# Kernel optimization log

Hardware: AMD Instinct MI355X
Metric: run time of the kernel (lower is better)

Reference implementation:

```python
import jax, jax.numpy as jnp
import numpy as np

MD_S = 1
MD_R = 16
EVAL_STEPS = 7
INV_T = 100.0
EPS = 1e-6

B, C, S = 16, 512, 4096  # batch, channels, flattened spatial


def setup_inputs() -> dict:
    key = jax.random.key(0)
    k1, k2 = jax.random.split(key)
    x = jax.random.uniform(k1, (B, C, S), dtype=jnp.float32)  # non-negative input for NMF
    bases = jax.random.uniform(k2, (B * MD_S, S, MD_R), dtype=jnp.float32)
    # F.normalize(bases, dim=1)
    bases = bases / (jnp.linalg.norm(bases, axis=1, keepdims=True) + 1e-12)
    return {"x": x, "bases": bases}


def _nmf_step(xm, bases, coef):
    # xm: (BS, D, N), bases: (BS, D, R), coef: (BS, N, R)
    # multiplicative update for coef
    num = jnp.einsum('bdn,bdr->bnr', xm, bases)
    den = jnp.einsum('bnr,brs->bns', coef, jnp.einsum('bdr,bds->brs', bases, bases))
    coef = coef * num / (den + EPS)
    # multiplicative update for bases
    num = jnp.einsum('bdn,bnr->bdr', xm, coef)
    den = jnp.einsum('bdr,brs->bds', bases, jnp.einsum('bnr,bns->brs', coef, coef))
    bases = bases * num / (den + EPS)
    return bases, coef


def _local_inference(xm, bases):
    # coef init: softmax(inv_t * x^T bases)
    coef = jax.nn.softmax(INV_T * jnp.einsum('bdn,bdr->bnr', xm, bases), axis=-1)

    def body(carry, _):
        b, c = _nmf_step(xm, carry[0], carry[1])
        return (b, c), None

    (bases, coef), _ = jax.lax.scan(body, (bases, coef), None, length=EVAL_STEPS)
    return bases, coef


def reference(x, bases):
    Bb, Cc, Ss = x.shape
    D = Ss
    N = Cc // MD_S
    xm = x.reshape(Bb * MD_S, N, D).transpose(0, 2, 1)  # (BS, D, N)

    bases_i, coef_i = jax.lax.stop_gradient(_local_inference(xm, bases))

    # compute_coef (differentiable in the original module)
    num = jnp.einsum('bdn,bdr->bnr', xm, bases_i)
    den = jnp.einsum('bnr,brs->bns', coef_i, jnp.einsum('bdr,bds->brs', bases_i, bases_i))
    coef = coef_i * num / (den + EPS)

    # x_rec = bases @ coef^T -> (BS, D, N) -> transpose -> (B, C, S)
    out = jnp.einsum('bdr,bnr->bdn', bases_i, coef)
    out = out.transpose(0, 2, 1).reshape(Bb, Cc, Ss)
    return out
```

## Files before the change

kernel.cpp:

```cpp
#include <hip/hip_runtime.h>

#define EPS 1e-6f

template <int CTRL>
__device__ __forceinline__ float dpp_add(float v) {
  int moved = __builtin_amdgcn_update_dpp(0, __float_as_int(v), CTRL, 0xF, 0xF, false);
  return v + __int_as_float(moved);
}

__global__ __launch_bounds__(512, 4) void kernelA(
    const float* __restrict__ x, const float* __restrict__ bases,
    float* __restrict__ Ppart, float* __restrict__ CtC)
{
  __shared__ __align__(16) float lb[512 * 20];
  const int tid = threadIdx.x;
  const int grp = blockIdx.x;
  const int b = blockIdx.y;
  const int h = blockIdx.z;
  if (h == 0 && grp == 0 && tid < 256) CtC[b * 256 + tid] = 0.0f;
  const int w = tid >> 6;
  const int lane = tid & 63;
  const int rg = w & 3;
  const int rh = w >> 2;
  const int n0 = grp * 32 + rg * 8;
  const float* __restrict__ xp = x + ((size_t)(b * 512 + n0)) * 4096 + h * 2048;
  const float4* __restrict__ srcf4 =
      (const float4*)(bases + ((size_t)(b * 4096 + h * 2048)) * 16);

  float acc[8][8];
#pragma unroll
  for (int i = 0; i < 8; ++i)
#pragma unroll
    for (int r = 0; r < 8; ++r) acc[i][r] = 0.0f;

  for (int c = 0; c < 4; ++c) {
#pragma unroll
    for (int k = 0; k < 4; ++k) {
      int idx = k * 512 + tid;
      int dl = idx >> 2, q = idx & 3;
      *(float4*)(&lb[dl * 20 + q * 4]) = srcf4[(c * 512 + dl) * 4 + q];
    }
    __syncthreads();
    const float* __restrict__ xpc = xp + c * 512;
#pragma unroll
    for (int j = 0; j < 8; ++j) {
      const int dl = j * 64 + lane;
      float4 b0 = *(const float4*)(&lb[dl * 20 + rh * 8]);
      float4 b1 = *(const float4*)(&lb[dl * 20 + rh * 8 + 4]);
      float xv[8];
#pragma unroll
      for (int i = 0; i < 8; ++i) xv[i] = xpc[(size_t)i * 4096 + dl];
#pragma unroll
      for (int i = 0; i < 8; ++i) {
        acc[i][0] = fmaf(xv[i], b0.x, acc[i][0]);
        acc[i][1] = fmaf(xv[i], b0.y, acc[i][1]);
        acc[i][2] = fmaf(xv[i], b0.z, acc[i][2]);
        acc[i][3] = fmaf(xv[i], b0.w, acc[i][3]);
        acc[i][4] = fmaf(xv[i], b1.x, acc[i][4]);
        acc[i][5] = fmaf(xv[i], b1.y, acc[i][5]);
        acc[i][6] = fmaf(xv[i], b1.z, acc[i][6]);
        acc[i][7] = fmaf(xv[i], b1.w, acc[i][7]);
      }
    }
    __syncthreads();
  }

#pragma unroll
  for (int i = 0; i < 8; ++i)
#pragma unroll
    for (int r = 0; r < 8; ++r) {
      float v = acc[i][r];
      v = dpp_add<0x121>(v);
      v = dpp_add<0x122>(v);
      v = dpp_add<0x124>(v);
      v = dpp_add<0x128>(v);
      v += __shfl_xor(v, 16, 64);
      v += __shfl_xor(v, 32, 64);
      acc[i][r] = v;
    }

  if (lane == 0) {
    float* __restrict__ pp =
        Ppart + (((size_t)(h * 16 + b)) * 512 + n0) * 16 + rh * 8;
#pragma unroll
    for (int i = 0; i < 8; ++i) {
      *(float4*)(pp + i * 16) = make_float4(acc[i][0], acc[i][1], acc[i][2], acc[i][3]);
      *(float4*)(pp + i * 16 + 4) = make_float4(acc[i][4], acc[i][5], acc[i][6], acc[i][7]);
    }
  }
}

__global__ __launch_bounds__(256) void kernelSM(
    const float* __restrict__ Ppart, float* __restrict__ coef)
{
  const int gid = blockIdx.x * 256 + threadIdx.x;
  const int b = gid >> 9, n = gid & 511;
  const float* __restrict__ p0 = Ppart + (((size_t)b) * 512 + n) * 16;
  const float* __restrict__ p1 = Ppart + (((size_t)(16 + b)) * 512 + n) * 16;
  float p[16];
#pragma unroll
  for (int r = 0; r < 16; ++r) p[r] = p0[r] + p1[r];
  float m = p[0];
#pragma unroll
  for (int r = 1; r < 16; ++r) m = fmaxf(m, p[r]);
  float e[16];
  float s = 0.0f;
#pragma unroll
  for (int r = 0; r < 16; ++r) { e[r] = __expf(100.0f * (p[r] - m)); s += e[r]; }
  float inv = 1.0f / s;
  float* __restrict__ crow = coef + (((size_t)b) * 512 + n) * 16;
#pragma unroll
  for (int r = 0; r < 16; ++r) crow[r] = e[r] * inv;
}

__global__ __launch_bounds__(256) void kernelGram(
    const float* __restrict__ M, float* __restrict__ out, int L)
{
  __shared__ __align__(16) float sm[256 * 20];
  __shared__ __align__(16) float part[4 * 272];
  const int tid = threadIdx.x;
  const int b = blockIdx.y;
  const int sl = blockIdx.x;
  const float4* __restrict__ src = (const float4*)(M + ((size_t)b * L + (size_t)sl * 256) * 16);
#pragma unroll
  for (int k = 0; k < 4; ++k) {
    int idx = k * 256 + tid;
    int row = idx >> 2, q = idx & 3;
    *(float4*)(&sm[row * 20 + q * 4]) = src[idx];
  }
  __syncthreads();
  const int rq = tid & 3;
  const int s = (tid >> 2) & 15;
  const int g = tid >> 6;
  float a0 = 0.f, a1 = 0.f, a2 = 0.f, a3 = 0.f;
#pragma unroll 4
  for (int l = g * 64; l < g * 64 + 64; ++l) {
    float4 bv = *(const float4*)(&sm[l * 20 + rq * 4]);
    float cs = sm[l * 20 + s];
    a0 = fmaf(cs, bv.x, a0);
    a1 = fmaf(cs, bv.y, a1);
    a2 = fmaf(cs, bv.z, a2);
    a3 = fmaf(cs, bv.w, a3);
  }
  *(float4*)(&part[g * 272 + s * 16 + rq * 4]) = make_float4(a0, a1, a2, a3);
  __syncthreads();
  float v = part[0 * 272 + tid] + part[1 * 272 + tid] + part[2 * 272 + tid] + part[3 * 272 + tid];
  atomicAdd(out + b * 256 + tid, v);
}

__global__ __launch_bounds__(256) void kernelCU(
    float* __restrict__ coef, const float* __restrict__ Ppart,
    const float* __restrict__ BtBr, float* __restrict__ BtBz,
    float* __restrict__ CtCadd)
{
  __shared__ __align__(16) float sm[256 * 20 + 4 * 272];
  const int tid = threadIdx.x;
  BtBz[blockIdx.x * 128 + (tid & 127)] = 0.0f;
  const int b = blockIdx.x >> 1;
  const int n = ((blockIdx.x & 1) << 8) + tid;
  float* __restrict__ crow = coef + ((size_t)(b * 512 + n)) * 16;
  const float* __restrict__ p0 = Ppart + (((size_t)b) * 512 + n) * 16;
  const float* __restrict__ p1 = Ppart + (((size_t)(16 + b)) * 512 + n) * 16;
  const float* __restrict__ btb = BtBr + b * 256;
  float cv[16], den[16];
#pragma unroll
  for (int r = 0; r < 16; ++r) cv[r] = crow[r];
#pragma unroll
  for (int r = 0; r < 16; ++r) den[r] = 0.f;
#pragma unroll
  for (int s2 = 0; s2 < 16; ++s2) {
    const float bs = cv[s2];
#pragma unroll
    for (int r = 0; r < 16; ++r) den[r] = fmaf(bs, btb[s2 * 16 + r], den[r]);
  }
#pragma unroll
  for (int r = 0; r < 16; ++r) {
    float cn = cv[r] * (p0[r] + p1[r]) / (den[r] + EPS);
    crow[r] = cn;
    sm[tid * 20 + r] = cn;
  }
  __syncthreads();
  const int rq = tid & 3;
  const int s = (tid >> 2) & 15;
  const int g = tid >> 6;
  float a0 = 0.f, a1 = 0.f, a2 = 0.f, a3 = 0.f;
#pragma unroll 4
  for (int l = g * 64; l < g * 64 + 64; ++l) {
    float4 bv = *(const float4*)(&sm[l * 20 + rq * 4]);
    float cs = sm[l * 20 + s];
    a0 = fmaf(cs, bv.x, a0);
    a1 = fmaf(cs, bv.y, a1);
    a2 = fmaf(cs, bv.z, a2);
    a3 = fmaf(cs, bv.w, a3);
  }
  float* part = sm + 5120;
  *(float4*)(&part[g * 272 + s * 16 + rq * 4]) = make_float4(a0, a1, a2, a3);
  __syncthreads();
  float v = part[0 * 272 + tid] + part[1 * 272 + tid] + part[2 * 272 + tid] + part[3 * 272 + tid];
  atomicAdd(CtCadd + b * 256 + tid, v);
}

__global__ __launch_bounds__(256) void kernelBacc(
    const float* __restrict__ x, const float* __restrict__ coef,
    float* __restrict__ qpart)
{
  const int tid = threadIdx.x;
  const int dt = blockIdx.x, ns = blockIdx.y, b = blockIdx.z;
  const int d = dt * 256 + tid;
  const float* __restrict__ xp = x + ((size_t)(b * 512 + ns * 128)) * 4096 + d;
  const float* __restrict__ cp = coef + ((size_t)(b * 512 + ns * 128)) * 16;
  float acc[16];
#pragma unroll
  for (int r = 0; r < 16; ++r) acc[r] = 0.f;
#pragma unroll 4
  for (int n = 0; n < 128; ++n) {
    const float xv = xp[(size_t)n * 4096];
    const float* __restrict__ crow = cp + n * 16;
#pragma unroll
    for (int r = 0; r < 16; ++r) acc[r] = fmaf(xv, crow[r], acc[r]);
  }
  float* __restrict__ qp = qpart + (((size_t)(ns * 16 + b)) * 4096 + d) * 16;
#pragma unroll
  for (int q = 0; q < 4; ++q)
    *(float4*)(qp + q * 4) = make_float4(acc[q * 4], acc[q * 4 + 1], acc[q * 4 + 2], acc[q * 4 + 3]);
}

__global__ __launch_bounds__(256) void kernelBfin(
    const float* __restrict__ qpart, float* __restrict__ bases,
    const float* __restrict__ CtC, float* __restrict__ BtBadd)
{
  __shared__ __align__(16) float sm[256 * 20 + 4 * 272];
  const int tid = threadIdx.x;
  const int dt = blockIdx.x, b = blockIdx.y;
  const int d = dt * 256 + tid;
  float acc[16];
#pragma unroll
  for (int r = 0; r < 16; ++r) acc[r] = 0.f;
#pragma unroll
  for (int ns = 0; ns < 4; ++ns) {
    const float* __restrict__ qp = qpart + (((size_t)(ns * 16 + b)) * 4096 + d) * 16;
#pragma unroll
    for (int q = 0; q < 4; ++q) {
      float4 v = *(const float4*)(qp + q * 4);
      acc[q * 4 + 0] += v.x; acc[q * 4 + 1] += v.y; acc[q * 4 + 2] += v.z; acc[q * 4 + 3] += v.w;
    }
  }
  float* __restrict__ brow = bases + ((size_t)(b * 4096 + d)) * 16;
  float bv[16];
#pragma unroll
  for (int r = 0; r < 16; ++r) bv[r] = brow[r];
  const float* __restrict__ ctc = CtC + b * 256;
  float den[16];
#pragma unroll
  for (int r = 0; r < 16; ++r) den[r] = 0.f;
#pragma unroll
  for (int s2 = 0; s2 < 16; ++s2) {
    const float bs = bv[s2];
#pragma unroll
    for (int r = 0; r < 16; ++r) den[r] = fmaf(bs, ctc[s2 * 16 + r], den[r]);
  }
#pragma unroll
  for (int r = 0; r < 16; ++r) {
    float bn = bv[r] * acc[r] / (den[r] + EPS);
    brow[r] = bn;
    sm[tid * 20 + r] = bn;
  }
  __syncthreads();
  const int rq = tid & 3;
  const int s = (tid >> 2) & 15;
  const int g = tid >> 6;
  float a0 = 0.f, a1 = 0.f, a2 = 0.f, a3 = 0.f;
#pragma unroll 4
  for (int l = g * 64; l < g * 64 + 64; ++l) {
    float4 bq = *(const float4*)(&sm[l * 20 + rq * 4]);
    float cs = sm[l * 20 + s];
    a0 = fmaf(cs, bq.x, a0);
    a1 = fmaf(cs, bq.y, a1);
    a2 = fmaf(cs, bq.z, a2);
    a3 = fmaf(cs, bq.w, a3);
  }
  float* part = sm + 5120;
  *(float4*)(&part[g * 272 + s * 16 + rq * 4]) = make_float4(a0, a1, a2, a3);
  __syncthreads();
  float v = part[0 * 272 + tid] + part[1 * 272 + tid] + part[2 * 272 + tid] + part[3 * 272 + tid];
  atomicAdd(BtBadd + b * 256 + tid, v);
}

__global__ __launch_bounds__(256) void kernelOut(
    const float* __restrict__ bases, const float* __restrict__ coef,
    float* __restrict__ out)
{
  const int tid = threadIdx.x;
  const int dt = blockIdx.x, ns = blockIdx.y, b = blockIdx.z;
  const int d0 = dt * 1024 + tid * 4;
  float bv[4][16];
#pragma unroll
  for (int k = 0; k < 4; ++k) {
    const float* __restrict__ brow = bases + ((size_t)(b * 4096 + d0 + k)) * 16;
#pragma unroll
    for (int r = 0; r < 16; ++r) bv[k][r] = brow[r];
  }
  const float* __restrict__ cp = coef + ((size_t)(b * 512 + ns * 32)) * 16;
  float* __restrict__ op = out + ((size_t)(b * 512 + ns * 32)) * 4096 + d0;
#pragma unroll 4
  for (int n = 0; n < 32; ++n) {
    const float* __restrict__ crow = cp + n * 16;
    float v[4];
#pragma unroll
    for (int k = 0; k < 4; ++k) {
      float s = 0.f;
#pragma unroll
      for (int r = 0; r < 16; ++r) s = fmaf(bv[k][r], crow[r], s);
      v[k] = s;
    }
    *(float4*)(op + (size_t)n * 4096) = make_float4(v[0], v[1], v[2], v[3]);
  }
}

extern "C" void kernel_launch(void* const* d_in, const int* in_sizes, int n_in,
                              void* d_out, int out_size, void* d_ws, size_t ws_size,
                              hipStream_t stream) {
  const float* x = (const float*)d_in[0];
  const float* bases_in = (const float*)d_in[1];
  float* out = (float*)d_out;
  float* ws = (float*)d_ws;

  float* bases = ws;
  float* coef  = bases + 1048576;
  float* Ppart = coef + 131072;
  float* btb0  = Ppart + 262144;
  float* btb1  = btb0 + 4096;
  float* ctc   = btb1 + 4096;
  float* qpart = ctc + 4096;
  float* btb[2] = {btb0, btb1};

  hipMemsetAsync(btb0, 0, 4096 * sizeof(float), stream);
  hipMemcpyAsync(bases, bases_in, 1048576 * sizeof(float),
                 hipMemcpyDeviceToDevice, stream);

  kernelA<<<dim3(16, 16, 2), 512, 0, stream>>>(x, bases, Ppart, ctc);
  kernelSM<<<32, 256, 0, stream>>>(Ppart, coef);
  kernelGram<<<dim3(16, 16), 256, 0, stream>>>(bases, btb0, 4096);

  for (int t = 0; t < 7; ++t) {
    if (t > 0) kernelA<<<dim3(16, 16, 2), 512, 0, stream>>>(x, bases, Ppart, ctc);
    kernelCU<<<32, 256, 0, stream>>>(coef, Ppart, btb[t & 1], btb[(t + 1) & 1], ctc);
    kernelBacc<<<dim3(16, 4, 16), 256, 0, stream>>>(x, coef, qpart);
    kernelBfin<<<dim3(16, 16), 256, 0, stream>>>(qpart, bases, ctc, btb[(t + 1) & 1]);
  }

  kernelA<<<dim3(16, 16, 2), 512, 0, stream>>>(x, bases, Ppart, ctc);
  kernelCU<<<32, 256, 0, stream>>>(coef, Ppart, btb[1], btb[0], ctc);
  kernelOut<<<dim3(4, 16, 16), 256, 0, stream>>>(bases, coef, out);
}
```

Before: 1.009 ms.

## Retile x^T·bases kernel with float4 x loads and widen Bacc to two columns

kernelA moves from 512-thread blocks (each wave covering 8 rows and 8 of the 16 ranks) to 256-thread blocks where each wave covers 4 rows and all 16 ranks. Each lane now reads x as float4 over 4 consecutive d values, and the bases tile sits in an unpadded 16-float-stride LDS layout with a rotation swizzle to avoid bank conflicts. kernelBacc now has each thread handle two adjacent d columns via float2 loads, which halves the grid and reuses each coef row for two columns. The intent is wider, more coalesced global loads and fewer LDS/coef reads per FMA, at the cost of more registers per thread in kernelBacc.

```diff
diff --git a/kernel.cpp b/kernel.cpp
--- a/kernel.cpp
+++ b/kernel.cpp
@@ -8,67 +8,85 @@
   return v + __int_as_float(moved);
 }
 
-__global__ __launch_bounds__(512, 4) void kernelA(
+__global__ __launch_bounds__(256, 4) void kernelA(
     const float* __restrict__ x, const float* __restrict__ bases,
     float* __restrict__ Ppart, float* __restrict__ CtC)
 {
-  __shared__ __align__(16) float lb[512 * 20];
+  __shared__ __align__(16) float lb[512 * 16];
   const int tid = threadIdx.x;
   const int grp = blockIdx.x;
   const int b = blockIdx.y;
   const int h = blockIdx.z;
-  if (h == 0 && grp == 0 && tid < 256) CtC[b * 256 + tid] = 0.0f;
+  if (h == 0 && grp == 0) CtC[b * 256 + tid] = 0.0f;
   const int w = tid >> 6;
   const int lane = tid & 63;
-  const int rg = w & 3;
-  const int rh = w >> 2;
-  const int n0 = grp * 32 + rg * 8;
+  const int rot = lane & 3;
+  const int n0 = grp * 16 + w * 4;
   const float* __restrict__ xp = x + ((size_t)(b * 512 + n0)) * 4096 + h * 2048;
   const float4* __restrict__ srcf4 =
       (const float4*)(bases + ((size_t)(b * 4096 + h * 2048)) * 16);
 
-  float acc[8][8];
-#pragma unroll
-  for (int i = 0; i < 8; ++i)
-#pragma unroll
-    for (int r = 0; r < 8; ++r) acc[i][r] = 0.0f;
+  float acc[4][16];
+#pragma unroll
+  for (int i = 0; i < 4; ++i)
+#pragma unroll
+    for (int r = 0; r < 16; ++r) acc[i][r] = 0.0f;
 
   for (int c = 0; c < 4; ++c) {
 #pragma unroll
-    for (int k = 0; k < 4; ++k) {
-      int idx = k * 512 + tid;
+    for (int k = 0; k < 8; ++k) {
+      int idx = k * 256 + tid;
       int dl = idx >> 2, q = idx & 3;
-      *(float4*)(&lb[dl * 20 + q * 4]) = srcf4[(c * 512 + dl) * 4 + q];
+      int pos = ((q + (dl >> 2)) & 3) * 4;
+      *(float4*)(&lb[dl * 16 + pos]) = srcf4[(c * 512 + dl) * 4 + q];
     }
     __syncthreads();
     const float* __restrict__ xpc = xp + c * 512;
 #pragma unroll
-    for (int j = 0; j < 8; ++j) {
-      const int dl = j * 64 + lane;
-      float4 b0 = *(const float4*)(&lb[dl * 20 + rh * 8]);
-      float4 b1 = *(const float4*)(&lb[dl * 20 + rh * 8 + 4]);
-      float xv[8];
-#pragma unroll
-      for (int i = 0; i < 8; ++i) xv[i] = xpc[(size_t)i * 4096 + dl];
-#pragma unroll
-      for (int i = 0; i < 8; ++i) {
-        acc[i][0] = fmaf(xv[i], b0.x, acc[i][0]);
-        acc[i][1] = fmaf(xv[i], b0.y, acc[i][1]);
-        acc[i][2] = fmaf(xv[i], b0.z, acc[i][2]);
-        acc[i][3] = fmaf(xv[i], b0.w, acc[i][3]);
-        acc[i][4] = fmaf(xv[i], b1.x, acc[i][4]);
-        acc[i][5] = fmaf(xv[i], b1.y, acc[i][5]);
-        acc[i][6] = fmaf(xv[i], b1.z, acc[i][6]);
-        acc[i][7] = fmaf(xv[i], b1.w, acc[i][7]);
+    for (int j = 0; j < 2; ++j) {
+      const int d0 = j * 256 + lane * 4;
+      float xr[4][4];
+#pragma unroll
+      for (int i = 0; i < 4; ++i) {
+        float4 t = *(const float4*)(xpc + (size_t)i * 4096 + d0);
+        xr[i][0] = t.x; xr[i][1] = t.y; xr[i][2] = t.z; xr[i][3] = t.w;
       }
+#pragma unroll
+      for (int k = 0; k < 4; ++k) {
+        const float* __restrict__ br = &lb[(d0 + k) * 16];
+        float4 bq0 = *(const float4*)(br + (((0 + rot) & 3) * 4));
+        float4 bq1 = *(const float4*)(br + (((1 + rot) & 3) * 4));
+        float4 bq2 = *(const float4*)(br + (((2 + rot) & 3) * 4));
+        float4 bq3 = *(const float4*)(br + (((3 + rot) & 3) * 4));
+#pragma unroll
+        for (int i = 0; i < 4; ++i) {
+          const float xf = xr[i][k];
+          acc[i][0]  = fmaf(xf, bq0.x, acc[i][0]);
+          acc[i][1]  = fmaf(xf, bq0.y, acc[i][1]);
+          acc[i][2]  = fmaf(xf, bq0.z, acc[i][2]);
+          acc[i][3]  = fmaf(xf, bq0.w, acc[i][3]);
+          acc[i][4]  = fmaf(xf, bq1.x, acc[i][4]);
+          acc[i][5]  = fmaf(xf, bq1.y, acc[i][5]);
+          acc[i][6]  = fmaf(xf, bq1.z, acc[i][6]);
+          acc[i][7]  = fmaf(xf, bq1.w, acc[i][7]);
+          acc[i][8]  = fmaf(xf, bq2.x, acc[i][8]);
+          acc[i][9]  = fmaf(xf, bq2.y, acc[i][9]);
+          acc[i][10] = fmaf(xf, bq2.z, acc[i][10]);
+          acc[i][11] = fmaf(xf, bq2.w, acc[i][11]);
+          acc[i][12] = fmaf(xf, bq3.x, acc[i][12]);
+          acc[i][13] = fmaf(xf, bq3.y, acc[i][13]);
+          acc[i][14] = fmaf(xf, bq3.z, acc[i][14]);
+          acc[i][15] = fmaf(xf, bq3.w, acc[i][15]);
+        }
+      }
     }
     __syncthreads();
   }
 
 #pragma unroll
-  for (int i = 0; i < 8; ++i)
-#pragma unroll
-    for (int r = 0; r < 8; ++r) {
+  for (int i = 0; i < 4; ++i)
+#pragma unroll
+    for (int r = 0; r < 16; ++r) {
       float v = acc[i][r];
       v = dpp_add<0x121>(v);
       v = dpp_add<0x122>(v);
@@ -81,11 +99,13 @@
 
   if (lane == 0) {
     float* __restrict__ pp =
-        Ppart + (((size_t)(h * 16 + b)) * 512 + n0) * 16 + rh * 8;
-#pragma unroll
-    for (int i = 0; i < 8; ++i) {
-      *(float4*)(pp + i * 16) = make_float4(acc[i][0], acc[i][1], acc[i][2], acc[i][3]);
-      *(float4*)(pp + i * 16 + 4) = make_float4(acc[i][4], acc[i][5], acc[i][6], acc[i][7]);
+        Ppart + (((size_t)(h * 16 + b)) * 512 + n0) * 16;
+#pragma unroll
+    for (int i = 0; i < 4; ++i) {
+#pragma unroll
+      for (int q = 0; q < 4; ++q)
+        *(float4*)(pp + i * 16 + q * 4) =
+            make_float4(acc[i][q * 4], acc[i][q * 4 + 1], acc[i][q * 4 + 2], acc[i][q * 4 + 3]);
     }
   }
 }
@@ -206,23 +226,29 @@
 {
   const int tid = threadIdx.x;
   const int dt = blockIdx.x, ns = blockIdx.y, b = blockIdx.z;
-  const int d = dt * 256 + tid;
+  const int d = dt * 512 + tid * 2;
   const float* __restrict__ xp = x + ((size_t)(b * 512 + ns * 128)) * 4096 + d;
   const float* __restrict__ cp = coef + ((size_t)(b * 512 + ns * 128)) * 16;
-  float acc[16];
-#pragma unroll
-  for (int r = 0; r < 16; ++r) acc[r] = 0.f;
+  float acc[2][16];
+#pragma unroll
+  for (int r = 0; r < 16; ++r) { acc[0][r] = 0.f; acc[1][r] = 0.f; }
 #pragma unroll 4
   for (int n = 0; n < 128; ++n) {
-    const float xv = xp[(size_t)n * 4096];
+    const float2 xv = *(const float2*)(xp + (size_t)n * 4096);
     const float* __restrict__ crow = cp + n * 16;
 #pragma unroll
-    for (int r = 0; r < 16; ++r) acc[r] = fmaf(xv, crow[r], acc[r]);
+    for (int r = 0; r < 16; ++r) {
+      acc[0][r] = fmaf(xv.x, crow[r], acc[0][r]);
+      acc[1][r] = fmaf(xv.y, crow[r], acc[1][r]);
+    }
   }
   float* __restrict__ qp = qpart + (((size_t)(ns * 16 + b)) * 4096 + d) * 16;
 #pragma unroll
   for (int q = 0; q < 4; ++q)
-    *(float4*)(qp + q * 4) = make_float4(acc[q * 4], acc[q * 4 + 1], acc[q * 4 + 2], acc[q * 4 + 3]);
+    *(float4*)(qp + q * 4) = make_float4(acc[0][q * 4], acc[0][q * 4 + 1], acc[0][q * 4 + 2], acc[0][q * 4 + 3]);
+#pragma unroll
+  for (int q = 0; q < 4; ++q)
+    *(float4*)(qp + 16 + q * 4) = make_float4(acc[1][q * 4], acc[1][q * 4 + 1], acc[1][q * 4 + 2], acc[1][q * 4 + 3]);
 }
 
 __global__ __launch_bounds__(256) void kernelBfin(
@@ -338,18 +364,18 @@
   hipMemcpyAsync(bases, bases_in, 1048576 * sizeof(float),
                  hipMemcpyDeviceToDevice, stream);
 
-  kernelA<<<dim3(16, 16, 2), 512, 0, stream>>>(x, bases, Ppart, ctc);
+  kernelA<<<dim3(32, 16, 2), 256, 0, stream>>>(x, bases, Ppart, ctc);
   kernelSM<<<32, 256, 0, stream>>>(Ppart, coef);
   kernelGram<<<dim3(16, 16), 256, 0, stream>>>(bases, btb0, 4096);
 
   for (int t = 0; t < 7; ++t) {
-    if (t > 0) kernelA<<<dim3(16, 16, 2), 512, 0, stream>>>(x, bases, Ppart, ctc);
+    if (t > 0) kernelA<<<dim3(32, 16, 2), 256, 0, stream>>>(x, bases, Ppart, ctc);
     kernelCU<<<32, 256, 0, stream>>>(coef, Ppart, btb[t & 1], btb[(t + 1) & 1], ctc);
-    kernelBacc<<<dim3(16, 4, 16), 256, 0, stream>>>(x, coef, qpart);
+    kernelBacc<<<dim3(8, 4, 16), 256, 0, stream>>>(x, coef, qpart);
     kernelBfin<<<dim3(16, 16), 256, 0, stream>>>(qpart, bases, ctc, btb[(t + 1) & 1]);
   }
 
-  kernelA<<<dim3(16, 16, 2), 512, 0, stream>>>(x, bases, Ppart, ctc);
+  kernelA<<<dim3(32, 16, 2), 256, 0, stream>>>(x, bases, Ppart, ctc);
   kernelCU<<<32, 256, 0, stream>>>(coef, Ppart, btb[1], btb[0], ctc);
   kernelOut<<<dim3(4, 16, 16), 256, 0, stream>>>(bases, coef, out);
 }
```

Result: slower. 1.043 ms (+3.3%).
